# Optimization experiments

Measured on AMD Instinct MI355X. Metric: run time of the kernel, lower is better.

Reference implementation:

```python
import jax, jax.numpy as jnp
import numpy as np

N = 50000
E = 800000
D = 128
EPS = 1e-5


def setup_inputs() -> dict:
    key = jax.random.key(0)
    ks = jax.random.split(key, 8)
    scale = 1.0 / np.sqrt(D)
    x = jax.random.normal(ks[0], (N, D), dtype=jnp.float32)
    edge_index = jax.random.randint(ks[1], (2, E), 0, N, dtype=jnp.int64)
    return {
        "x": x,
        "edge_index": edge_index,
        "W1l": jax.random.normal(ks[2], (D, D), dtype=jnp.float32) * scale,
        "b1": jnp.zeros((D,), jnp.float32),
        "W1r": jax.random.normal(ks[3], (D, D), dtype=jnp.float32) * scale,
        "g1": jnp.ones((D,), jnp.float32),
        "bt1": jnp.zeros((D,), jnp.float32),
        "W2l": jax.random.normal(ks[4], (D, D), dtype=jnp.float32) * scale,
        "b2": jnp.zeros((D,), jnp.float32),
        "W2r": jax.random.normal(ks[5], (D, D), dtype=jnp.float32) * scale,
        "g2": jnp.ones((D,), jnp.float32),
        "bt2": jnp.zeros((D,), jnp.float32),
    }


def _sage(x, src, dst, Wl, b, Wr):
    # mean aggregation of source features at destination nodes
    agg = jax.ops.segment_sum(x[src], dst, num_segments=N)  # [N, D]
    deg = jax.ops.segment_sum(jnp.ones((E,), x.dtype), dst, num_segments=N)
    agg = agg / jnp.maximum(deg, 1.0)[:, None]
    # PyG SAGEConv: lin_l(agg) + bias + lin_r(x) (root, no bias)
    return agg @ Wl + b + x @ Wr


def _bn(h, g, bt):
    # training-mode batch norm over node dim
    mu = jnp.mean(h, axis=0)
    var = jnp.var(h, axis=0)
    return (h - mu) * (g / jnp.sqrt(var + EPS)) + bt


def reference(x, edge_index, W1l, b1, W1r, g1, bt1, W2l, b2, W2r, g2, bt2):
    src, dst = edge_index[0], edge_index[1]
    h = _sage(x, src, dst, W1l, b1, W1r)
    h = jax.nn.relu(_bn(h, g1, bt1))
    # dropout = identity (eval mode)
    h = _sage(h, src, dst, W2l, b2, W2r)
    h = _bn(h, g2, bt2)
    # residual (in_channels == out_channels -> identity skip)
    return jax.nn.relu(h + x)
```

## Files before the change

### kernel.cpp

```cpp
#include <hip/hip_runtime.h>

typedef unsigned short u16;
typedef unsigned char u8;
typedef __attribute__((ext_vector_type(8))) short short8;
typedef __attribute__((ext_vector_type(2))) float f32x2;
typedef __attribute__((ext_vector_type(4))) float f32x4;
typedef __attribute__((ext_vector_type(4))) int i32x4;
typedef __attribute__((ext_vector_type(4))) unsigned short us4;
typedef __attribute__((ext_vector_type(8))) unsigned short us8;
typedef __attribute__((ext_vector_type(4))) unsigned int u32x4;

#define N_NODES 50000
#define N_EDGES 800000
#define DIM 128
#define NINV (1.0f / 50000.0f)
#define SROW 136
#define NBKT 3125
#define CAP 512

__device__ __forceinline__ float bf2f(u16 u) {
    union { unsigned int i; float f; } v; v.i = ((unsigned int)u) << 16; return v.f;
}
__device__ __forceinline__ u16 f2bf(float f) {
    union { float f; unsigned int i; } v; v.f = f;
    return (u16)((v.i + 0x7FFFu + ((v.i >> 16) & 1u)) >> 16);
}

__global__ __launch_bounds__(256) void k_prep(
        const float* __restrict__ W1l, const float* __restrict__ W1r, u16* __restrict__ Bp1,
        const float* __restrict__ W2l, const float* __restrict__ W2r, u16* __restrict__ Bp2,
        const float* __restrict__ x, u16* __restrict__ xh, u8* __restrict__ xf8,
        const int* __restrict__ esrc, const int* __restrict__ edst,
        int* __restrict__ bcnt, unsigned* __restrict__ bucket, int splitB) {
    int b = blockIdx.x;
    if (b < 32) {
        const float* Wl = (b < 16) ? W1l : W2l;
        const float* Wr = (b < 16) ? W1r : W2r;
        u16* Bp = (b < 16) ? Bp1 : Bp2;
        int idx = (b & 15) * 256 + threadIdx.x;
        int lane = idx & 63;
        int kc = (idx >> 6) & 7;
        int nt = idx >> 9;
        int q = lane >> 4, nn = lane & 15;
        int col = nt * 16 + nn;
        #pragma unroll
        for (int j = 0; j < 8; ++j) {
            int k = kc * 32 + q * 8 + j;
            float v = (k < 128) ? Wl[k * 128 + col] : Wr[(k - 128) * 128 + col];
            Bp[(long)idx * 8 + j] = f2bf(v);
        }
    } else if (b < 32 + splitB) {
        long i4 = ((long)(b - 32) * 256 + threadIdx.x) * 4;
        f32x4 v = *(const f32x4*)(x + i4);
        us4 h;
        #pragma unroll
        for (int j = 0; j < 4; ++j) h[j] = f2bf(v[j]);
        *(us4*)(xh + i4) = h;
        int p = __builtin_amdgcn_cvt_pk_fp8_f32(v[0], v[1], 0, false);
        p = __builtin_amdgcn_cvt_pk_fp8_f32(v[2], v[3], p, true);
        *(int*)(xf8 + i4) = p;
    } else {
        int e4 = (b - 32 - splitB) * 1024 + threadIdx.x * 4;
        if (e4 < N_EDGES) {
            i32x4 d4 = *(const i32x4*)(edst + e4);
            i32x4 s4 = *(const i32x4*)(esrc + e4);
            #pragma unroll
            for (int j = 0; j < 4; ++j) {
                int d = d4[j];
                int key = d >> 4;
                int pos = atomicAdd(&bcnt[key << 4], 1);
                if (pos < CAP)
                    bucket[(long)key * CAP + pos] = ((unsigned)s4[j] << 4) | (unsigned)(d & 15);
            }
        }
    }
}

__global__ __launch_bounds__(256) void k_sort(
        const int* __restrict__ bcnt, const unsigned* __restrict__ bucket,
        u16* __restrict__ col_srt, u16* __restrict__ hdr) {
    __shared__ int sHist[16], sStart[16], sCur[16];
    __shared__ u16 sSort[CAP];
    int tid = threadIdx.x;
    int bid = blockIdx.x;
    int cnt = bcnt[bid << 4]; if (cnt > CAP) cnt = CAP;
    bool h0 = tid < cnt, h1 = tid + 256 < cnt;
    unsigned e0 = 0u, e1 = 0u;
    if (h0) e0 = bucket[(long)bid * CAP + tid];
    if (h1) e1 = bucket[(long)bid * CAP + tid + 256];
    if (tid < 16) sHist[tid] = 0;
    __syncthreads();
    if (h0) atomicAdd(&sHist[e0 & 15u], 1);
    if (h1) atomicAdd(&sHist[e1 & 15u], 1);
    __syncthreads();
    if (tid == 0) {
        int acc = 0;
        #pragma unroll
        for (int i = 0; i < 16; ++i) { sStart[i] = acc; sCur[i] = acc; acc += sHist[i]; }
    }
    __syncthreads();
    if (h0) { int p = atomicAdd(&sCur[e0 & 15u], 1); sSort[p] = (u16)(e0 >> 4); }
    if (h1) { int p = atomicAdd(&sCur[e1 & 15u], 1); sSort[p] = (u16)(e1 >> 4); }
    __syncthreads();
    if (h0) col_srt[(long)bid * CAP + tid] = sSort[tid];
    if (h1) col_srt[(long)bid * CAP + tid + 256] = sSort[tid + 256];
    if (tid < 16) {
        hdr[bid * 32 + tid] = (u16)sStart[tid];
        hdr[bid * 32 + 16 + tid] = (u16)sHist[tid];
    }
}

template<int BN>
__device__ __forceinline__ void acc_row16(u32x4 w,
        float sum[16], const float av[16], const float ov[16]) {
    float t[16];
    f32x2 p;
    #pragma unroll
    for (int h = 0; h < 4; ++h) {
        p = __builtin_amdgcn_cvt_pk_f32_fp8((int)w[h], false); t[h*4+0] = p[0]; t[h*4+1] = p[1];
        p = __builtin_amdgcn_cvt_pk_f32_fp8((int)w[h], true);  t[h*4+2] = p[0]; t[h*4+3] = p[1];
    }
    #pragma unroll
    for (int k = 0; k < 16; ++k) {
        float v = t[k];
        if (BN) { v = v * av[k] + ov[k]; v = v > 0.f ? v : 0.f; }
        sum[k] += v;
    }
}

template<int BN, int W8>
__global__ __launch_bounds__(256) void k_ag(
        const u8* __restrict__ fq, const u16* __restrict__ fh,
        const u16* __restrict__ hdr, const u16* __restrict__ col_srt,
        const u16* __restrict__ Bph, const float* __restrict__ bias,
        const float* __restrict__ statsPrev, const float* __restrict__ gP,
        const float* __restrict__ btP,
        u16* __restrict__ h16, u8* __restrict__ h8, float* __restrict__ stats) {
    __shared__ u16 sA[16 * SROW];
    __shared__ float acS[256];
    int tid = threadIdx.x;
    long nodebase = (long)blockIdx.x * 16;

    if (BN) {
        if (tid < 128) {
            float s = 0.f, qq = 0.f;
            #pragma unroll
            for (int b = 0; b < 8; ++b) {
                s  += statsPrev[b * 512 + tid];
                qq += statsPrev[b * 512 + 256 + tid];
            }
            float mu = s * NINV;
            float var = qq * NINV - mu * mu;
            float a = gP[tid] * rsqrtf(var + 1e-5f);
            acS[tid] = a;
            acS[128 + tid] = btP[tid] - mu * a;
        }
        __syncthreads();
    }

    {
        int grp = tid >> 4;
        int g   = tid & 15;
        int sub = g >> 3;
        int gl  = g & 7;
        int d16 = gl * 16;
        const u16* cs = col_srt + (long)blockIdx.x * CAP;
        int st  = hdr[blockIdx.x * 32 + grp];
        int deg = hdr[blockIdx.x * 32 + 16 + grp];
        int s = st, e = st + deg;
        float av[16], ov[16];
        if (BN) {
            #pragma unroll
            for (int k = 0; k < 16; ++k) { av[k] = acS[d16 + k]; ov[k] = acS[128 + d16 + k]; }
        }
        float sum[16];
        #pragma unroll
        for (int k = 0; k < 16; ++k) sum[k] = 0.f;
        int j = s + sub;
        for (; j + 6 < e; j += 8) {
            int i0 = cs[j], i1 = cs[j + 2], i2 = cs[j + 4], i3 = cs[j + 6];
            u32x4 w0 = *(const u32x4*)(fq + (long)i0 * DIM + d16);
            u32x4 w1 = *(const u32x4*)(fq + (long)i1 * DIM + d16);
            u32x4 w2 = *(const u32x4*)(fq + (long)i2 * DIM + d16);
            u32x4 w3 = *(const u32x4*)(fq + (long)i3 * DIM + d16);
            acc_row16<BN>(w0, sum, av, ov);
            acc_row16<BN>(w1, sum, av, ov);
            acc_row16<BN>(w2, sum, av, ov);
            acc_row16<BN>(w3, sum, av, ov);
        }
        for (; j < e; j += 2) {
            int i0 = cs[j];
            u32x4 w0 = *(const u32x4*)(fq + (long)i0 * DIM + d16);
            acc_row16<BN>(w0, sum, av, ov);
        }
        #pragma unroll
        for (int k = 0; k < 16; ++k) sum[k] += __shfl_xor(sum[k], 8);
        if (sub == 0) {
            float dn = (deg > 0) ? 1.f / (float)deg : 1.f;
            us8 r0, r1;
            #pragma unroll
            for (int k = 0; k < 8; ++k) {
                r0[k] = f2bf(sum[k] * dn);
                r1[k] = f2bf(sum[8 + k] * dn);
            }
            *(us8*)(sA + grp * SROW + d16) = r0;
            *(us8*)(sA + grp * SROW + d16 + 8) = r1;
        }
    }
    __syncthreads();

    int cg = tid >> 6, lane = tid & 63;
    int q = lane >> 4, nn = lane & 15;
    long rc = nodebase + nn;

    short8 ah[8];
    #pragma unroll
    for (int kc = 0; kc < 4; ++kc)
        ah[kc] = *(const short8*)(sA + nn * SROW + kc * 32 + q * 8);
    #pragma unroll
    for (int kc = 0; kc < 4; ++kc) {
        int ko = kc * 32 + q * 8;
        us8 rv = *(const us8*)(fh + rc * DIM + ko);
        short8 t;
        if (BN) {
            #pragma unroll
            for (int j = 0; j < 8; ++j) {
                float v = bf2f(rv[j]) * acS[ko + j] + acS[128 + ko + j];
                t[j] = (short)f2bf(v > 0.f ? v : 0.f);
            }
        } else {
            #pragma unroll
            for (int j = 0; j < 8; ++j) t[j] = (short)rv[j];
        }
        ah[4 + kc] = t;
    }

    f32x4 acc[2];
    acc[0] = (f32x4){0.f, 0.f, 0.f, 0.f};
    acc[1] = (f32x4){0.f, 0.f, 0.f, 0.f};

    #pragma unroll
    for (int kc = 0; kc < 8; ++kc) {
        #pragma unroll
        for (int nt = 0; nt < 2; ++nt) {
            int ntg = cg * 2 + nt;
            short8 bh = *(const short8*)(Bph + (((ntg * 8 + kc) * 64 + lane) << 3));
            acc[nt] = __builtin_amdgcn_mfma_f32_16x16x32_bf16(ah[kc], bh, acc[nt], 0, 0, 0);
        }
    }

    int bank = blockIdx.x & 7;
    #pragma unroll
    for (int nt = 0; nt < 2; ++nt) {
        int col = cg * 32 + nt * 16 + nn;
        float bv = bias[col];
        float ps = 0.f, pq = 0.f;
        #pragma unroll
        for (int r = 0; r < 4; ++r) {
            float v = acc[nt][r] + bv;
            long idx = (nodebase + q * 4 + r) * DIM + col;
            h16[idx] = f2bf(v);
            if (W8) {
                int pb = __builtin_amdgcn_cvt_pk_fp8_f32(v, v, 0, false);
                h8[idx] = (u8)(pb & 0xff);
            }
            ps += v; pq += v * v;
        }
        ps += __shfl_xor(ps, 16);
        ps += __shfl_xor(ps, 32);
        pq += __shfl_xor(pq, 16);
        pq += __shfl_xor(pq, 32);
        if (q == 0) {
            atomicAdd(&stats[bank * 512 + col], ps);
            atomicAdd(&stats[bank * 512 + 256 + col], pq);
        }
    }
}

__global__ __launch_bounds__(256) void k_bn_add_relu(
        const u16* __restrict__ h, const float* __restrict__ stats,
        const float* __restrict__ g, const float* __restrict__ bt,
        const float* __restrict__ x, float* __restrict__ outv) {
    __shared__ float acS[256];
    int tid = threadIdx.x;
    if (tid < 128) {
        float s = 0.f, qq = 0.f;
        #pragma unroll
        for (int b = 0; b < 8; ++b) {
            s  += stats[b * 512 + tid];
            qq += stats[b * 512 + 256 + tid];
        }
        float mu = s * NINV;
        float var = qq * NINV - mu * mu;
        float a = g[tid] * rsqrtf(var + 1e-5f);
        acS[tid] = a;
        acS[128 + tid] = bt[tid] - mu * a;
    }
    __syncthreads();
    long i8 = ((long)blockIdx.x * 256 + tid) * 8;
    int c = (int)(i8 & 127);
    us8 hv = *(const us8*)(h + i8);
    f32x4 x0 = *(const f32x4*)(x + i8);
    f32x4 x1 = *(const f32x4*)(x + i8 + 4);
    f32x4 r0, r1;
    #pragma unroll
    for (int j = 0; j < 4; ++j) {
        float v = bf2f(hv[j]) * acS[c + j] + acS[128 + c + j] + x0[j];
        r0[j] = v > 0.f ? v : 0.f;
        float w = bf2f(hv[4 + j]) * acS[c + 4 + j] + acS[128 + c + 4 + j] + x1[j];
        r1[j] = w > 0.f ? w : 0.f;
    }
    *(f32x4*)(outv + i8) = r0;
    *(f32x4*)(outv + i8 + 4) = r1;
}

extern "C" void kernel_launch(void* const* d_in, const int* in_sizes, int n_in,
                              void* d_out, int out_size, void* d_ws, size_t ws_size,
                              hipStream_t stream) {
    (void)in_sizes; (void)n_in; (void)out_size; (void)ws_size;
    const float* x   = (const float*)d_in[0];
    const int*   ei  = (const int*)d_in[1];
    const float* W1l = (const float*)d_in[2];
    const float* b1  = (const float*)d_in[3];
    const float* W1r = (const float*)d_in[4];
    const float* g1  = (const float*)d_in[5];
    const float* bt1 = (const float*)d_in[6];
    const float* W2l = (const float*)d_in[7];
    const float* b2  = (const float*)d_in[8];
    const float* W2r = (const float*)d_in[9];
    const float* g2  = (const float*)d_in[10];
    const float* bt2 = (const float*)d_in[11];
    float* out = (float*)d_out;

    const int* esrc = ei;
    const int* edst = ei + N_EDGES;

    char* ws = (char*)d_ws;
    size_t off = 0;
    auto alloc = [&](size_t bytes) { size_t p = off; off = (off + bytes + 255) & ~(size_t)255; return p; };
    float* stats1  = (float*)(ws + alloc(4096 * 4));
    float* stats2  = (float*)(ws + alloc(4096 * 4));
    int*   bcnt    = (int*)  (ws + alloc((size_t)NBKT * 16 * 4));
    size_t zero_bytes = off;
    unsigned* bucket = (unsigned*)(ws + alloc((size_t)NBKT * CAP * 4));
    u16*   col_srt = (u16*)  (ws + alloc((size_t)NBKT * CAP * 2));
    u16*   hdr     = (u16*)  (ws + alloc((size_t)NBKT * 32 * 2));
    u16*   xh      = (u16*)  (ws + alloc((size_t)N_NODES * DIM * 2));
    u8*    xf8     = (u8*)   (ws + alloc((size_t)N_NODES * DIM));
    u16*   hb1     = (u16*)  (ws + alloc((size_t)N_NODES * DIM * 2));
    u8*    h1f8    = (u8*)   (ws + alloc((size_t)N_NODES * DIM));
    u16*   hb2     = (u16*)  (ws + alloc((size_t)N_NODES * DIM * 2));
    u16*   Bp1h    = (u16*)  (ws + alloc(256 * 128 * 2));
    u16*   Bp2h    = (u16*)  (ws + alloc(256 * 128 * 2));

    hipMemsetAsync(ws, 0, zero_bytes, stream);

    const int AGB = N_NODES / 16;
    const int EWB4 = (int)(((long)N_NODES * DIM) / 1024);
    const int EWB8 = (int)(((long)N_NODES * DIM) / 2048);
    const int EDGB = (N_EDGES + 1023) / 1024;
    const int PREPB = 32 + EWB4 + EDGB;

    k_prep<<<PREPB, 256, 0, stream>>>(W1l, W1r, Bp1h, W2l, W2r, Bp2h, x, xh, xf8,
                                      esrc, edst, bcnt, bucket, EWB4);

    k_sort<<<NBKT, 256, 0, stream>>>(bcnt, bucket, col_srt, hdr);

    k_ag<0, 1><<<AGB, 256, 0, stream>>>(xf8, xh, hdr, col_srt, Bp1h, b1,
                                        stats1, g1, bt1, hb1, h1f8, stats1);

    k_ag<1, 0><<<AGB, 256, 0, stream>>>(h1f8, hb1, hdr, col_srt, Bp2h, b2,
                                        stats1, g1, bt1, hb2, h1f8, stats2);

    k_bn_add_relu<<<EWB8, 256, 0, stream>>>(hb2, stats2, g2, bt2, x, out);
}
```

Before: 232.7 us.

## Replace per-bucket global atomics with two-level block-local edge binning

Edge bucketing now bins each block's 1024 edges by 800-node super-segment in shared memory, reserving space with one global atomic per bin instead of one per edge. It then scatters into 63 large segment buffers. The sort kernel now runs one 512-thread block per super-segment, builds per-node histograms and offsets, and writes the CSR-like col_srt and hdr. The aggregation kernel also stages its column indices in shared memory instead of reading them from global memory in the inner loop. The sort kernel launches far fewer, heavier blocks, which may reduce parallelism, and it keeps 32 entries per thread in registers.

```diff
diff --git a/kernel.cpp b/kernel.cpp
--- a/kernel.cpp
+++ b/kernel.cpp
@@ -17,6 +17,9 @@
 #define SROW 136
 #define NBKT 3125
 #define CAP 512
+#define SUPN 800
+#define NSUP 63
+#define SEGCAP 16384
 
 __device__ __forceinline__ float bf2f(u16 u) {
     union { unsigned int i; float f; } v; v.i = ((unsigned int)u) << 16; return v.f;
@@ -31,7 +34,7 @@
         const float* __restrict__ W2l, const float* __restrict__ W2r, u16* __restrict__ Bp2,
         const float* __restrict__ x, u16* __restrict__ xh, u8* __restrict__ xf8,
         const int* __restrict__ esrc, const int* __restrict__ edst,
-        int* __restrict__ bcnt, unsigned* __restrict__ bucket, int splitB) {
+        int* __restrict__ segCnt, unsigned* __restrict__ segBuf, int splitB) {
     int b = blockIdx.x;
     if (b < 32) {
         const float* Wl = (b < 16) ? W1l : W2l;
@@ -60,53 +63,107 @@
         p = __builtin_amdgcn_cvt_pk_fp8_f32(v[2], v[3], p, true);
         *(int*)(xf8 + i4) = p;
     } else {
-        int e4 = (b - 32 - splitB) * 1024 + threadIdx.x * 4;
-        if (e4 < N_EDGES) {
+        __shared__ int sHistB[64], sScanB[64], sCurB[64], sBaseB[64];
+        __shared__ unsigned sStage[1024];
+        __shared__ u8 sBinOf[1024];
+        int tid = threadIdx.x;
+        int hb = b - 32 - splitB;
+        int e4 = hb * 1024 + tid * 4;
+        bool val = e4 < N_EDGES;
+        if (tid < 64) sHistB[tid] = 0;
+        __syncthreads();
+        unsigned ent[4]; int bin[4];
+        if (val) {
             i32x4 d4 = *(const i32x4*)(edst + e4);
             i32x4 s4 = *(const i32x4*)(esrc + e4);
             #pragma unroll
             for (int j = 0; j < 4; ++j) {
-                int d = d4[j];
-                int key = d >> 4;
-                int pos = atomicAdd(&bcnt[key << 4], 1);
-                if (pos < CAP)
-                    bucket[(long)key * CAP + pos] = ((unsigned)s4[j] << 4) | (unsigned)(d & 15);
-            }
-        }
-    }
-}
-
-__global__ __launch_bounds__(256) void k_sort(
-        const int* __restrict__ bcnt, const unsigned* __restrict__ bucket,
+                unsigned dd = (unsigned)d4[j];
+                int bi = (int)(dd / 800u);
+                bin[j] = bi;
+                ent[j] = ((unsigned)s4[j] << 10) | (dd - (unsigned)bi * 800u);
+                atomicAdd(&sHistB[bi], 1);
+            }
+        }
+        __syncthreads();
+        if (tid == 0) {
+            int acc = 0;
+            #pragma unroll
+            for (int i = 0; i < 64; ++i) { sScanB[i] = acc; sCurB[i] = acc; acc += sHistB[i]; }
+        }
+        __syncthreads();
+        if (val) {
+            #pragma unroll
+            for (int j = 0; j < 4; ++j) {
+                int p = atomicAdd(&sCurB[bin[j]], 1);
+                sStage[p] = ent[j];
+                sBinOf[p] = (u8)bin[j];
+            }
+        }
+        __syncthreads();
+        if (tid < 64) {
+            int c = sHistB[tid];
+            sBaseB[tid] = c ? atomicAdd(&segCnt[tid << 4], c) : 0;
+        }
+        __syncthreads();
+        int tcount = sScanB[63] + sHistB[63];
+        for (int p = tid; p < tcount; p += 256) {
+            int bn = sBinOf[p];
+            long ofs = (long)sBaseB[bn] + (p - sScanB[bn]);
+            if (ofs < SEGCAP)
+                segBuf[(long)bn * SEGCAP + ofs] = sStage[p];
+        }
+    }
+}
+
+__global__ __launch_bounds__(512) void k_sort(
+        const int* __restrict__ segCnt, const unsigned* __restrict__ segBuf,
         u16* __restrict__ col_srt, u16* __restrict__ hdr) {
-    __shared__ int sHist[16], sStart[16], sCur[16];
-    __shared__ u16 sSort[CAP];
+    __shared__ int sHist[SUPN], sStart[SUPN], sCur[SUPN];
     int tid = threadIdx.x;
-    int bid = blockIdx.x;
-    int cnt = bcnt[bid << 4]; if (cnt > CAP) cnt = CAP;
-    bool h0 = tid < cnt, h1 = tid + 256 < cnt;
-    unsigned e0 = 0u, e1 = 0u;
-    if (h0) e0 = bucket[(long)bid * CAP + tid];
-    if (h1) e1 = bucket[(long)bid * CAP + tid + 256];
-    if (tid < 16) sHist[tid] = 0;
-    __syncthreads();
-    if (h0) atomicAdd(&sHist[e0 & 15u], 1);
-    if (h1) atomicAdd(&sHist[e1 & 15u], 1);
-    __syncthreads();
-    if (tid == 0) {
-        int acc = 0;
-        #pragma unroll
-        for (int i = 0; i < 16; ++i) { sStart[i] = acc; sCur[i] = acc; acc += sHist[i]; }
-    }
-    __syncthreads();
-    if (h0) { int p = atomicAdd(&sCur[e0 & 15u], 1); sSort[p] = (u16)(e0 >> 4); }
-    if (h1) { int p = atomicAdd(&sCur[e1 & 15u], 1); sSort[p] = (u16)(e1 >> 4); }
-    __syncthreads();
-    if (h0) col_srt[(long)bid * CAP + tid] = sSort[tid];
-    if (h1) col_srt[(long)bid * CAP + tid + 256] = sSort[tid + 256];
-    if (tid < 16) {
-        hdr[bid * 32 + tid] = (u16)sStart[tid];
-        hdr[bid * 32 + 16 + tid] = (u16)sHist[tid];
+    int s = blockIdx.x;
+    int nnodes = N_NODES - s * SUPN; if (nnodes > SUPN) nnodes = SUPN;
+    int ngroups = nnodes >> 4;
+    int n = segCnt[s << 4]; if (n > SEGCAP) n = SEGCAP;
+    for (int i = tid; i < SUPN; i += 512) { sHist[i] = 0; sCur[i] = 0; }
+    __syncthreads();
+    const unsigned* seg = segBuf + (long)s * SEGCAP;
+    unsigned ent[32];
+    #pragma unroll
+    for (int i = 0; i < 32; ++i) {
+        int idx = i * 512 + tid;
+        ent[i] = (idx < n) ? seg[idx] : 0xFFFFFFFFu;
+    }
+    #pragma unroll
+    for (int i = 0; i < 32; ++i)
+        if (ent[i] != 0xFFFFFFFFu) atomicAdd(&sHist[ent[i] & 1023u], 1);
+    __syncthreads();
+    if (tid < ngroups) {
+        int base = 0;
+        int gb = (s * 50 + tid) * 32;
+        #pragma unroll
+        for (int i = 0; i < 16; ++i) {
+            int node = tid * 16 + i;
+            int d = sHist[node];
+            int st_c = base < CAP ? base : CAP;
+            int en_c = base + d < CAP ? base + d : CAP;
+            sStart[node] = base;
+            hdr[gb + i] = (u16)st_c;
+            hdr[gb + 16 + i] = (u16)(en_c - st_c);
+            base += d;
+        }
+    }
+    __syncthreads();
+    #pragma unroll
+    for (int i = 0; i < 32; ++i) {
+        unsigned e = ent[i];
+        if (e != 0xFFFFFFFFu) {
+            int node = (int)(e & 1023u);
+            int pos = atomicAdd(&sCur[node], 1);
+            int ofs = sStart[node] + pos;
+            if (ofs < CAP)
+                col_srt[(long)(s * 50 + (node >> 4)) * CAP + ofs] = (u16)(e >> 10);
+        }
     }
 }
 
@@ -138,8 +195,12 @@
         u16* __restrict__ h16, u8* __restrict__ h8, float* __restrict__ stats) {
     __shared__ u16 sA[16 * SROW];
     __shared__ float acS[256];
+    __shared__ __align__(16) u16 sIdx[CAP];
     int tid = threadIdx.x;
     long nodebase = (long)blockIdx.x * 16;
+
+    if (tid < 64)
+        *(us8*)(sIdx + tid * 8) = *(const us8*)(col_srt + (long)blockIdx.x * CAP + tid * 8);
 
     if (BN) {
         if (tid < 128) {
@@ -155,8 +216,8 @@
             acS[tid] = a;
             acS[128 + tid] = btP[tid] - mu * a;
         }
-        __syncthreads();
-    }
+    }
+    __syncthreads();
 
     {
         int grp = tid >> 4;
@@ -164,7 +225,6 @@
         int sub = g >> 3;
         int gl  = g & 7;
         int d16 = gl * 16;
-        const u16* cs = col_srt + (long)blockIdx.x * CAP;
         int st  = hdr[blockIdx.x * 32 + grp];
         int deg = hdr[blockIdx.x * 32 + 16 + grp];
         int s = st, e = st + deg;
@@ -178,7 +238,7 @@
         for (int k = 0; k < 16; ++k) sum[k] = 0.f;
         int j = s + sub;
         for (; j + 6 < e; j += 8) {
-            int i0 = cs[j], i1 = cs[j + 2], i2 = cs[j + 4], i3 = cs[j + 6];
+            int i0 = sIdx[j], i1 = sIdx[j + 2], i2 = sIdx[j + 4], i3 = sIdx[j + 6];
             u32x4 w0 = *(const u32x4*)(fq + (long)i0 * DIM + d16);
             u32x4 w1 = *(const u32x4*)(fq + (long)i1 * DIM + d16);
             u32x4 w2 = *(const u32x4*)(fq + (long)i2 * DIM + d16);
@@ -189,7 +249,7 @@
             acc_row16<BN>(w3, sum, av, ov);
         }
         for (; j < e; j += 2) {
-            int i0 = cs[j];
+            int i0 = sIdx[j];
             u32x4 w0 = *(const u32x4*)(fq + (long)i0 * DIM + d16);
             acc_row16<BN>(w0, sum, av, ov);
         }
@@ -340,9 +400,9 @@
     auto alloc = [&](size_t bytes) { size_t p = off; off = (off + bytes + 255) & ~(size_t)255; return p; };
     float* stats1  = (float*)(ws + alloc(4096 * 4));
     float* stats2  = (float*)(ws + alloc(4096 * 4));
-    int*   bcnt    = (int*)  (ws + alloc((size_t)NBKT * 16 * 4));
+    int*   segCnt  = (int*)  (ws + alloc(64 * 16 * 4));
     size_t zero_bytes = off;
-    unsigned* bucket = (unsigned*)(ws + alloc((size_t)NBKT * CAP * 4));
+    unsigned* segBuf = (unsigned*)(ws + alloc((size_t)NSUP * SEGCAP * 4));
     u16*   col_srt = (u16*)  (ws + alloc((size_t)NBKT * CAP * 2));
     u16*   hdr     = (u16*)  (ws + alloc((size_t)NBKT * 32 * 2));
     u16*   xh      = (u16*)  (ws + alloc((size_t)N_NODES * DIM * 2));
@@ -362,9 +422,9 @@
     const int PREPB = 32 + EWB4 + EDGB;
 
     k_prep<<<PREPB, 256, 0, stream>>>(W1l, W1r, Bp1h, W2l, W2r, Bp2h, x, xh, xf8,
-                                      esrc, edst, bcnt, bucket, EWB4);
-
-    k_sort<<<NBKT, 256, 0, stream>>>(bcnt, bucket, col_srt, hdr);
+                                      esrc, edst, segCnt, segBuf, EWB4);
+
+    k_sort<<<NSUP, 512, 0, stream>>>(segCnt, segBuf, col_srt, hdr);
 
     k_ag<0, 1><<<AGB, 256, 0, stream>>>(xf8, xh, hdr, col_srt, Bp1h, b1,
                                         stats1, g1, bt1, hb1, h1f8, stats1);
```

Result: faster. 207.1 us (-11.0%).
